# Optimization experiments

Hardware: AMD Instinct MI355X
Metric: run time of the kernel (lower is better)

The kernel has to match this reference:

```python
import jax, jax.numpy as jnp
import numpy as np
import math

B, T, D = 2, 2048, 4096
H, HD = 32, 128  # n_head, head_dim; H*HD == D
THETA = 10000.0


def _rope_tables(T, hd, theta):
    # standard RoPE: freqs_i = theta^(-2i/hd), angle[t,i] = t * freqs_i
    inv = 1.0 / (theta ** (np.arange(0, hd, 2, dtype=np.float32) / hd))  # [hd/2]
    ang = np.arange(T, dtype=np.float32)[:, None] * inv[None, :]          # [T, hd/2]
    return jnp.asarray(np.cos(ang)), jnp.asarray(np.sin(ang))


def setup_inputs() -> dict:
    key = jax.random.key(0)
    ks = jax.random.split(key, 5)
    scale = 1.0 / math.sqrt(D)
    x = jax.random.normal(ks[0], (B, T, D), dtype=jnp.float32)
    Wq = jax.random.normal(ks[1], (D, H * HD), dtype=jnp.float32) * scale
    Wk = jax.random.normal(ks[2], (D, H * HD), dtype=jnp.float32) * scale
    Wv = jax.random.normal(ks[3], (D, H * HD), dtype=jnp.float32) * scale
    Wo = jax.random.normal(ks[4], (D, D), dtype=jnp.float32) * scale
    fc, fs = _rope_tables(T, HD, THETA)
    return {"x": x, "freqs_cos": fc, "freqs_sin": fs,
            "Wq": Wq, "Wk": Wk, "Wv": Wv, "Wo": Wo}


def _apply_rope(t, cos, sin):
    # t: [B, T, H, HD]; complex rotation on interleaved (even, odd) pairs
    tp = t.reshape(*t.shape[:-1], HD // 2, 2)
    xr, xi = tp[..., 0], tp[..., 1]
    c = cos[None, :, None, :]  # [1, T, 1, HD/2]
    s = sin[None, :, None, :]
    out_r = xr * c - xi * s
    out_i = xr * s + xi * c
    return jnp.stack([out_r, out_i], axis=-1).reshape(t.shape)


def reference(x, freqs_cos, freqs_sin, Wq, Wk, Wv, Wo):
    Bc, Tc, _ = x.shape
    q = (x @ Wq).reshape(Bc, Tc, H, HD)
    k = (x @ Wk).reshape(Bc, Tc, H, HD)
    v = (x @ Wv).reshape(Bc, Tc, H, HD)
    q = _apply_rope(q, freqs_cos, freqs_sin)
    k = _apply_rope(k, freqs_cos, freqs_sin)
    scale = 1.0 / math.sqrt(HD)
    scores = jnp.einsum('bqhd,bkhd->bhqk', q, k) * scale  # [B,H,T,T]
    causal = jnp.tril(jnp.ones((Tc, Tc), dtype=bool))
    scores = jnp.where(causal[None, None], scores, -jnp.inf)
    attn = jax.nn.softmax(scores, axis=-1)
    y = jnp.einsum('bhqk,bkhd->bqhd', attn, v).reshape(Bc, Tc, H * HD)
    return y @ Wo
```

## Files before the change

### kernel.cpp

```cpp
#include <hip/hip_runtime.h>

typedef unsigned short ushort_t;
typedef unsigned int uint32;

typedef float f32x4 __attribute__((ext_vector_type(4)));
typedef __bf16 bf16x8 __attribute__((ext_vector_type(8)));
typedef unsigned short us8 __attribute__((ext_vector_type(8)));
typedef unsigned short us4 __attribute__((ext_vector_type(4)));

#define TSEQ 2048
#define DMODEL 4096

__device__ __forceinline__ ushort_t f2bf(float f) {
  uint32 u = __builtin_bit_cast(uint32, f);
  u += 0x7FFFu + ((u >> 16) & 1u);
  return (ushort_t)(u >> 16);
}
__device__ __forceinline__ float bf2f(ushort_t u) {
  return __builtin_bit_cast(float, ((uint32)u) << 16);
}

__device__ __forceinline__ void gload_lds16(const void* g, void* l) {
  auto gp = (const __attribute__((address_space(1))) void*)g;
  auto lp = (__attribute__((address_space(3))) void*)l;
  __builtin_amdgcn_global_load_lds(gp, lp, 16, 0, 0);
}

__global__ __launch_bounds__(256) void k_cast_bf16(const float* __restrict__ in,
                                                   ushort_t* __restrict__ out, int n4) {
  int g = blockIdx.x * 256 + threadIdx.x;
  if (g >= n4) return;
  float4 v = *(const float4*)(in + (size_t)g * 4);
  us4 o; o[0] = f2bf(v.x); o[1] = f2bf(v.y); o[2] = f2bf(v.z); o[3] = f2bf(v.w);
  *(us4*)(out + (size_t)g * 4) = o;
}

__global__ __launch_bounds__(256) void k_transpose_cast4(const float* __restrict__ W0,
                                                         const float* __restrict__ W1,
                                                         const float* __restrict__ W2,
                                                         const float* __restrict__ W3,
                                                         ushort_t* __restrict__ WTbase) {
  __shared__ __align__(16) ushort_t ts[64 * 72];
  const float* Ws[4] = {W0, W1, W2, W3};
  const float* W = Ws[blockIdx.z];
  ushort_t* WT = WTbase + (size_t)blockIdx.z * DMODEL * DMODEL;
  const int tid = threadIdx.x;
  const int n0 = blockIdx.x * 64, k0 = blockIdx.y * 64;
  #pragma unroll
  for (int it = 0; it < 4; ++it) {
    int e = it * 256 + tid;
    int r = e >> 4, c4 = e & 15;
    float4 v = *(const float4*)(W + (size_t)(k0 + r) * DMODEL + n0 + c4 * 4);
    us4 o; o[0] = f2bf(v.x); o[1] = f2bf(v.y); o[2] = f2bf(v.z); o[3] = f2bf(v.w);
    *(us4*)&ts[r * 72 + c4 * 4] = o;
  }
  __syncthreads();
  #pragma unroll
  for (int it = 0; it < 4; ++it) {
    int e = it * 256 + tid;
    int r2 = e >> 4, c4 = e & 15;
    us4 o;
    #pragma unroll
    for (int j = 0; j < 4; ++j) o[j] = ts[(c4 * 4 + j) * 72 + r2];
    *(us4*)(WT + (size_t)(n0 + r2) * DMODEL + k0 + c4 * 4) = o;
  }
}

template <bool OUT_BF16, bool ROPE>
__global__ __launch_bounds__(256, 3)
void k_gemm128(const ushort_t* __restrict__ A, const ushort_t* __restrict__ Bt,
               void* __restrict__ Cv, int M, int N, int K,
               const float* __restrict__ fc, const float* __restrict__ fs) {
  __shared__ __align__(16) ushort_t As[128 * 32];
  __shared__ __align__(16) ushort_t Bs[128 * 32];
  const int tid = threadIdx.x;
  const int w = tid >> 6, l = tid & 63;
  const int wm = w >> 1, wn = w & 1;
  const int lg = l >> 4, lc = l & 15;

  const int nwg = gridDim.x;
  const int cpx = nwg >> 3;
  const int wg = (blockIdx.x & 7) * cpx + (blockIdx.x >> 3);
  const int nbn = N >> 7;
  const int bm = wg / nbn, bn = wg % nbn;

  const ushort_t* Ab = A + (size_t)(bm * 128) * K;
  const ushort_t* Bb = Bt + (size_t)(bn * 128) * K;

  const int csrc = (l & 3) ^ ((l >> 3) & 3);
  const ushort_t* gA[2]; const ushort_t* gB[2];
  int dstOff[2];
  #pragma unroll
  for (int j = 0; j < 2; ++j) {
    int row = w * 32 + j * 16 + (l >> 2);
    gA[j] = Ab + (size_t)row * K + csrc * 8;
    gB[j] = Bb + (size_t)row * K + csrc * 8;
    dstOff[j] = (w * 32 + j * 16) * 32;
  }

  int offA[4], offB[4];
  #pragma unroll
  for (int m = 0; m < 4; ++m)
    offA[m] = (wm * 64 + m * 16 + lc) * 32 + ((lg ^ ((lc >> 1) & 3)) * 8);
  #pragma unroll
  for (int n = 0; n < 4; ++n)
    offB[n] = (wn * 64 + n * 16 + lc) * 32 + ((lg ^ ((lc >> 1) & 3)) * 8);

  f32x4 acc[4][4];
  #pragma unroll
  for (int m = 0; m < 4; ++m)
    #pragma unroll
    for (int n = 0; n < 4; ++n) acc[m][n] = (f32x4){0.f, 0.f, 0.f, 0.f};

  const int NT = K >> 5;
  for (int t = 0; t < NT; ++t) {
    const int k0 = t << 5;
    __syncthreads();
    gload_lds16(gA[0] + k0, &As[dstOff[0]]);
    gload_lds16(gA[1] + k0, &As[dstOff[1]]);
    gload_lds16(gB[0] + k0, &Bs[dstOff[0]]);
    gload_lds16(gB[1] + k0, &Bs[dstOff[1]]);
    asm volatile("s_waitcnt vmcnt(0)" ::: "memory");
    __syncthreads();

    bf16x8 af[4], bfv[4];
    #pragma unroll
    for (int m = 0; m < 4; ++m) af[m] = *(const bf16x8*)&As[offA[m]];
    #pragma unroll
    for (int n = 0; n < 4; ++n) bfv[n] = *(const bf16x8*)&Bs[offB[n]];
    __builtin_amdgcn_s_setprio(1);
    #pragma unroll
    for (int m = 0; m < 4; ++m)
      #pragma unroll
      for (int n = 0; n < 4; ++n)
        acc[m][n] = __builtin_amdgcn_mfma_f32_16x16x32_bf16(af[m], bfv[n], acc[m][n], 0, 0, 0);
    __builtin_amdgcn_s_setprio(0);
  }

  #pragma unroll
  for (int m = 0; m < 4; ++m) {
    int row0 = bm * 128 + wm * 64 + m * 16 + lg * 4;
    #pragma unroll
    for (int n = 0; n < 4; ++n) {
      int col = bn * 128 + wn * 64 + n * 16 + lc;
      if (ROPE) {
        int i0 = (col & 127) >> 1;
        #pragma unroll
        for (int r = 0; r < 4; ++r) {
          int tt = (row0 + r) & (TSEQ - 1);
          float c = fc[tt * 64 + i0];
          float s = fs[tt * 64 + i0];
          float v = acc[m][n][r];
          float p = __shfl_xor(v, 1);
          float ov = (lc & 1) ? (p * s + v * c) : (v * c - p * s);
          ((ushort_t*)Cv)[(size_t)(row0 + r) * N + col] = f2bf(ov);
        }
      } else {
        #pragma unroll
        for (int r = 0; r < 4; ++r) {
          float v = acc[m][n][r];
          if (OUT_BF16) ((ushort_t*)Cv)[(size_t)(row0 + r) * N + col] = f2bf(v);
          else          ((float*)Cv)[(size_t)(row0 + r) * N + col] = v;
        }
      }
    }
  }
}

__global__ __launch_bounds__(512, 2)
void k_attn(const ushort_t* __restrict__ QK, const ushort_t* __restrict__ Vt,
            ushort_t* __restrict__ Y) {
  __shared__ __align__(16) ushort_t Ks[2][64 * 128];
  __shared__ __align__(16) ushort_t Vs[2][128 * 64];
  __shared__ __align__(16) ushort_t Ps[8][16 * 64];
  const int id = blockIdx.x;
  const int xcd = id & 7, slot = id >> 3;
  const int bx = slot & 7, gHi = slot >> 3;
  const int g = gHi * 8 + xcd;
  const int h = g & 31, b = g >> 5;
  const int tid = threadIdx.x;
  const int w = tid >> 6, l = tid & 63;
  const int lg = l >> 4, lc = l & 15;
  const float scale = 0.08838834764831845f;
  const float THR = 8.0f;
  const int QKS = 8192;

  auto stageKV = [&](int kv0, int buf) {
    #pragma unroll
    for (int i = 0; i < 2; ++i) {
      int seg = w * 2 + i;
      {
        int row = seg * 4 + (l >> 4);
        int csrc = (l & 15) ^ (row & 7);
        gload_lds16(QK + (size_t)(b * TSEQ + kv0 + row) * QKS + 4096 + h * 128 + csrc * 8,
                    &Ks[buf][seg * 512]);
      }
      {
        int row = seg * 8 + (l >> 3);
        int csrc = (l & 7) ^ (l >> 3);
        gload_lds16(Vt + (size_t)(h * 128 + row) * DMODEL + b * TSEQ + kv0 + csrc * 8,
                    &Vs[buf][seg * 512]);
      }
    }
  };

  for (int qi = 0; qi < 2; ++qi) {
    const int qt = qi ? (15 - bx) : bx;
    const int q0 = qt * 128;
    const int wrow0 = q0 + w * 16;

    bf16x8 qf[4];
    {
      const ushort_t* qp = QK + (size_t)(b * TSEQ + wrow0 + lc) * QKS + h * 128;
      #pragma unroll
      for (int ks = 0; ks < 4; ++ks) qf[ks] = *(const bf16x8*)(qp + ks * 32 + lg * 8);
    }

    float m_r[4], lp[4];
    #pragma unroll
    for (int r = 0; r < 4; ++r) { m_r[r] = -1e30f; lp[r] = 0.f; }
    f32x4 o[8];
    #pragma unroll
    for (int t = 0; t < 8; ++t) o[t] = (f32x4){0.f, 0.f, 0.f, 0.f};

    const int nkv = (qt + 1) * 2;
    stageKV(0, 0);
    for (int kt = 0; kt < nkv; ++kt) {
      const int cur = kt & 1;
      const int kv0 = kt * 64;
      if (kt + 1 < nkv) {
        stageKV((kt + 1) * 64, cur ^ 1);
        asm volatile("s_waitcnt vmcnt(4)" ::: "memory");
      } else {
        asm volatile("s_waitcnt vmcnt(0)" ::: "memory");
      }
      __builtin_amdgcn_s_barrier();

      if (kv0 <= wrow0 + 15) {
        f32x4 s[4];
        __builtin_amdgcn_s_setprio(1);
        #pragma unroll
        for (int n = 0; n < 4; ++n) {
          s[n] = (f32x4){0.f, 0.f, 0.f, 0.f};
          #pragma unroll
          for (int ks = 0; ks < 4; ++ks) {
            int row = n * 16 + lc;
            bf16x8 kf = *(const bf16x8*)&Ks[cur][row * 128 + ((ks * 32 + lg * 8) ^ ((row & 7) * 8))];
            s[n] = __builtin_amdgcn_mfma_f32_16x16x32_bf16(qf[ks], kf, s[n], 0, 0, 0);
          }
        }
        __builtin_amdgcn_s_setprio(0);

        float sv[4][4];
        if (kv0 + 63 > wrow0) {
          #pragma unroll
          for (int n = 0; n < 4; ++n)
            #pragma unroll
            for (int r = 0; r < 4; ++r) {
              float x = s[n][r] * scale;
              int kvg = kv0 + n * 16 + lc;
              int qg = wrow0 + lg * 4 + r;
              sv[n][r] = (kvg > qg) ? -1e30f : x;
            }
        } else {
          #pragma unroll
          for (int n = 0; n < 4; ++n)
            #pragma unroll
            for (int r = 0; r < 4; ++r) sv[n][r] = s[n][r] * scale;
        }

        float pmax[4];
        #pragma unroll
        for (int r = 0; r < 4; ++r)
          pmax[r] = fmaxf(fmaxf(sv[0][r], sv[1][r]), fmaxf(sv[2][r], sv[3][r]));
        bool ok = (pmax[0] <= m_r[0] + THR) && (pmax[1] <= m_r[1] + THR) &&
                  (pmax[2] <= m_r[2] + THR) && (pmax[3] <= m_r[3] + THR);
        if (!__all(ok)) {
          #pragma unroll
          for (int r = 0; r < 4; ++r) {
            float mx = pmax[r];
            #pragma unroll
            for (int off = 1; off < 16; off <<= 1) mx = fmaxf(mx, __shfl_xor(mx, off, 16));
            float mn = fmaxf(m_r[r], mx);
            float al = __expf(m_r[r] - mn);
            m_r[r] = mn;
            lp[r] *= al;
            #pragma unroll
            for (int t = 0; t < 8; ++t) o[t][r] *= al;
          }
        }

        #pragma unroll
        for (int n = 0; n < 4; ++n)
          #pragma unroll
          for (int r = 0; r < 4; ++r) {
            float p = __expf(sv[n][r] - m_r[r]);
            lp[r] += p;
            int row = lg * 4 + r, col = n * 16 + lc;
            Ps[w][row * 64 + (col ^ (lg * 16))] = f2bf(p);
          }

        __builtin_amdgcn_s_setprio(1);
        #pragma unroll
        for (int kvs = 0; kvs < 2; ++kvs) {
          bf16x8 pa = *(const bf16x8*)&Ps[w][lc * 64 + ((kvs * 32 + lg * 8) ^ ((lc >> 2) * 16))];
          #pragma unroll
          for (int t = 0; t < 8; ++t) {
            int vrow = t * 16 + lc;
            bf16x8 vb = *(const bf16x8*)&Vs[cur][vrow * 64 + ((kvs * 32 + lg * 8) ^ ((vrow & 7) * 8))];
            o[t] = __builtin_amdgcn_mfma_f32_16x16x32_bf16(pa, vb, o[t], 0, 0, 0);
          }
        }
        __builtin_amdgcn_s_setprio(0);
      }
      asm volatile("" ::: "memory");
      __builtin_amdgcn_s_barrier();
    }

    float linv[4];
    #pragma unroll
    for (int r = 0; r < 4; ++r) {
      float ls = lp[r];
      #pragma unroll
      for (int off = 1; off < 16; off <<= 1) ls += __shfl_xor(ls, off, 16);
      linv[r] = 1.0f / ls;
    }

    #pragma unroll
    for (int t = 0; t < 8; ++t)
      #pragma unroll
      for (int r = 0; r < 4; ++r) {
        int row = wrow0 + lg * 4 + r;
        int col = h * 128 + t * 16 + lc;
        Y[(size_t)(b * TSEQ + row) * DMODEL + col] = f2bf(o[t][r] * linv[r]);
      }
  }
}

extern "C" void kernel_launch(void* const* d_in, const int* in_sizes, int n_in,
                              void* d_out, int out_size, void* d_ws, size_t ws_size,
                              hipStream_t stream) {
  const float* x  = (const float*)d_in[0];
  const float* fc = (const float*)d_in[1];
  const float* fs = (const float*)d_in[2];
  const float* Wq = (const float*)d_in[3];
  const float* Wk = (const float*)d_in[4];
  const float* Wv = (const float*)d_in[5];
  const float* Wo = (const float*)d_in[6];

  const size_t SZ = (size_t)4096 * 4096;
  ushort_t* xb  = (ushort_t*)d_ws;
  ushort_t* WqT = xb + SZ;
  ushort_t* WkT = WqT + SZ;
  ushort_t* WvT = WkT + SZ;
  ushort_t* WoT = WvT + SZ;
  ushort_t* qk  = WoT + SZ;
  ushort_t* vT  = qk + 2 * SZ;
  ushort_t* yb  = vT + SZ;

  k_cast_bf16<<<16384, 256, 0, stream>>>(x, xb, 4194304);
  dim3 tg(64, 64, 4);
  k_transpose_cast4<<<tg, 256, 0, stream>>>(Wq, Wk, Wv, Wo, WqT);

  k_gemm128<true, true><<<2048, 256, 0, stream>>>(xb, WqT, qk, 4096, 8192, 4096, fc, fs);
  k_gemm128<true, false><<<1024, 256, 0, stream>>>(WvT, xb, vT, 4096, 4096, 4096, nullptr, nullptr);

  k_attn<<<512, 512, 0, stream>>>(qk, vT, yb);

  k_gemm128<false, false><<<1024, 256, 0, stream>>>(yb, WoT, d_out, 4096, 4096, 4096, nullptr, nullptr);
}
```

Before: 914.5 us.

## Double-buffer GEMM LDS with 128x256 tiles, 512 threads, split Q/K outputs

The GEMM kernel now uses 512-thread blocks computing 128x256 tiles with double-buffered LDS. The next K-slice load is issued before the current slice's MFMAs, so each iteration needs one barrier instead of two. The LDS swizzle also changes. The fused Q/K projection is split into two separate launches writing separate Q and K buffers, and the attention QK^T loop is reordered to iterate ks outermost. The aim is to hide global-load latency and raise data reuse per block, at the cost of more LDS per block and more launches.

```diff
diff --git a/kernel.cpp b/kernel.cpp
--- a/kernel.cpp
+++ b/kernel.cpp
@@ -67,67 +67,74 @@
 }
 
 template <bool OUT_BF16, bool ROPE>
-__global__ __launch_bounds__(256, 3)
-void k_gemm128(const ushort_t* __restrict__ A, const ushort_t* __restrict__ Bt,
-               void* __restrict__ Cv, int M, int N, int K,
-               const float* __restrict__ fc, const float* __restrict__ fs) {
-  __shared__ __align__(16) ushort_t As[128 * 32];
-  __shared__ __align__(16) ushort_t Bs[128 * 32];
+__global__ __launch_bounds__(512, 4)
+void k_gemm(const ushort_t* __restrict__ A, const ushort_t* __restrict__ Bt,
+            void* __restrict__ Cv, int M, int N, int K,
+            const float* __restrict__ fc, const float* __restrict__ fs) {
+  __shared__ __align__(16) ushort_t As[2][128 * 32];
+  __shared__ __align__(16) ushort_t Bs[2][256 * 32];
   const int tid = threadIdx.x;
   const int w = tid >> 6, l = tid & 63;
-  const int wm = w >> 1, wn = w & 1;
+  const int wr = w >> 2, wc = w & 3;
   const int lg = l >> 4, lc = l & 15;
 
   const int nwg = gridDim.x;
   const int cpx = nwg >> 3;
   const int wg = (blockIdx.x & 7) * cpx + (blockIdx.x >> 3);
-  const int nbn = N >> 7;
+  const int nbn = N >> 8;
   const int bm = wg / nbn, bn = wg % nbn;
 
   const ushort_t* Ab = A + (size_t)(bm * 128) * K;
-  const ushort_t* Bb = Bt + (size_t)(bn * 128) * K;
-
-  const int csrc = (l & 3) ^ ((l >> 3) & 3);
-  const ushort_t* gA[2]; const ushort_t* gB[2];
-  int dstOff[2];
-  #pragma unroll
-  for (int j = 0; j < 2; ++j) {
-    int row = w * 32 + j * 16 + (l >> 2);
-    gA[j] = Ab + (size_t)row * K + csrc * 8;
-    gB[j] = Bb + (size_t)row * K + csrc * 8;
-    dstOff[j] = (w * 32 + j * 16) * 32;
-  }
-
+  const ushort_t* Bb = Bt + (size_t)(bn * 256) * K;
+
+  const int slotA = tid;
+  const int rowA = slotA >> 2;
+  const int chA = (slotA & 3) ^ (rowA & 3) ^ (2 * ((rowA >> 2) & 1));
+  const ushort_t* gAp = Ab + (size_t)rowA * K + chA * 8;
+  const int dstA = (w * 64) * 8;
+
+  const int rowB0 = tid >> 2, rowB1 = (512 + tid) >> 2;
+  const int chB0 = (tid & 3) ^ (rowB0 & 3) ^ (2 * ((rowB0 >> 2) & 1));
+  const int chB1 = (tid & 3) ^ (rowB1 & 3) ^ (2 * ((rowB1 >> 2) & 1));
+  const ushort_t* gBp0 = Bb + (size_t)rowB0 * K + chB0 * 8;
+  const ushort_t* gBp1 = Bb + (size_t)rowB1 * K + chB1 * 8;
+  const int dstB0 = (w * 64) * 8;
+  const int dstB1 = (512 + w * 64) * 8;
+
+  const int rswz = (lg ^ (lc & 3) ^ (2 * ((lc >> 2) & 1))) * 8;
   int offA[4], offB[4];
   #pragma unroll
+  for (int m = 0; m < 4; ++m) offA[m] = (wr * 64 + m * 16 + lc) * 32 + rswz;
+  #pragma unroll
+  for (int n = 0; n < 4; ++n) offB[n] = (wc * 64 + n * 16 + lc) * 32 + rswz;
+
+  f32x4 acc[4][4];
+  #pragma unroll
   for (int m = 0; m < 4; ++m)
-    offA[m] = (wm * 64 + m * 16 + lc) * 32 + ((lg ^ ((lc >> 1) & 3)) * 8);
-  #pragma unroll
-  for (int n = 0; n < 4; ++n)
-    offB[n] = (wn * 64 + n * 16 + lc) * 32 + ((lg ^ ((lc >> 1) & 3)) * 8);
-
-  f32x4 acc[4][4];
-  #pragma unroll
-  for (int m = 0; m < 4; ++m)
     #pragma unroll
     for (int n = 0; n < 4; ++n) acc[m][n] = (f32x4){0.f, 0.f, 0.f, 0.f};
 
   const int NT = K >> 5;
+  auto stage = [&](int t, int buf) {
+    const int k0 = t << 5;
+    gload_lds16(gAp + k0, &As[buf][dstA]);
+    gload_lds16(gBp0 + k0, &Bs[buf][dstB0]);
+    gload_lds16(gBp1 + k0, &Bs[buf][dstB1]);
+  };
+
+  stage(0, 0);
+  asm volatile("s_waitcnt vmcnt(0)" ::: "memory");
+  __builtin_amdgcn_s_barrier();
+
   for (int t = 0; t < NT; ++t) {
-    const int k0 = t << 5;
-    __syncthreads();
-    gload_lds16(gA[0] + k0, &As[dstOff[0]]);
-    gload_lds16(gA[1] + k0, &As[dstOff[1]]);
-    gload_lds16(gB[0] + k0, &Bs[dstOff[0]]);
-    gload_lds16(gB[1] + k0, &Bs[dstOff[1]]);
-    asm volatile("s_waitcnt vmcnt(0)" ::: "memory");
-    __syncthreads();
+    const int cur = t & 1;
+    if (t + 1 < NT) stage(t + 1, cur ^ 1);
 
     bf16x8 af[4], bfv[4];
     #pragma unroll
-    for (int m = 0; m < 4; ++m) af[m] = *(const bf16x8*)&As[offA[m]];
-    #pragma unroll
-    for (int n = 0; n < 4; ++n) bfv[n] = *(const bf16x8*)&Bs[offB[n]];
+    for (int m = 0; m < 4; ++m) af[m] = *(const bf16x8*)&As[cur][offA[m]];
+    #pragma unroll
+    for (int n = 0; n < 4; ++n) bfv[n] = *(const bf16x8*)&Bs[cur][offB[n]];
     __builtin_amdgcn_s_setprio(1);
     #pragma unroll
     for (int m = 0; m < 4; ++m)
@@ -135,14 +142,19 @@
       for (int n = 0; n < 4; ++n)
         acc[m][n] = __builtin_amdgcn_mfma_f32_16x16x32_bf16(af[m], bfv[n], acc[m][n], 0, 0, 0);
     __builtin_amdgcn_s_setprio(0);
+
+    if (t + 1 < NT) {
+      asm volatile("s_waitcnt vmcnt(0)" ::: "memory");
+      __builtin_amdgcn_s_barrier();
+    }
   }
 
   #pragma unroll
   for (int m = 0; m < 4; ++m) {
-    int row0 = bm * 128 + wm * 64 + m * 16 + lg * 4;
+    int row0 = bm * 128 + wr * 64 + m * 16 + lg * 4;
     #pragma unroll
     for (int n = 0; n < 4; ++n) {
-      int col = bn * 128 + wn * 64 + n * 16 + lc;
+      int col = bn * 256 + wc * 64 + n * 16 + lc;
       if (ROPE) {
         int i0 = (col & 127) >> 1;
         #pragma unroll
@@ -168,8 +180,8 @@
 }
 
 __global__ __launch_bounds__(512, 2)
-void k_attn(const ushort_t* __restrict__ QK, const ushort_t* __restrict__ Vt,
-            ushort_t* __restrict__ Y) {
+void k_attn(const ushort_t* __restrict__ Q, const ushort_t* __restrict__ Kb,
+            const ushort_t* __restrict__ Vt, ushort_t* __restrict__ Y) {
   __shared__ __align__(16) ushort_t Ks[2][64 * 128];
   __shared__ __align__(16) ushort_t Vs[2][128 * 64];
   __shared__ __align__(16) ushort_t Ps[8][16 * 64];
@@ -183,7 +195,6 @@
   const int lg = l >> 4, lc = l & 15;
   const float scale = 0.08838834764831845f;
   const float THR = 8.0f;
-  const int QKS = 8192;
 
   auto stageKV = [&](int kv0, int buf) {
     #pragma unroll
@@ -192,7 +203,7 @@
       {
         int row = seg * 4 + (l >> 4);
         int csrc = (l & 15) ^ (row & 7);
-        gload_lds16(QK + (size_t)(b * TSEQ + kv0 + row) * QKS + 4096 + h * 128 + csrc * 8,
+        gload_lds16(Kb + (size_t)(b * TSEQ + kv0 + row) * DMODEL + h * 128 + csrc * 8,
                     &Ks[buf][seg * 512]);
       }
       {
@@ -211,7 +222,7 @@
 
     bf16x8 qf[4];
     {
-      const ushort_t* qp = QK + (size_t)(b * TSEQ + wrow0 + lc) * QKS + h * 128;
+      const ushort_t* qp = Q + (size_t)(b * TSEQ + wrow0 + lc) * DMODEL + h * 128;
       #pragma unroll
       for (int ks = 0; ks < 4; ++ks) qf[ks] = *(const bf16x8*)(qp + ks * 32 + lg * 8);
     }
@@ -238,17 +249,17 @@
 
       if (kv0 <= wrow0 + 15) {
         f32x4 s[4];
+        #pragma unroll
+        for (int n = 0; n < 4; ++n) s[n] = (f32x4){0.f, 0.f, 0.f, 0.f};
         __builtin_amdgcn_s_setprio(1);
         #pragma unroll
-        for (int n = 0; n < 4; ++n) {
-          s[n] = (f32x4){0.f, 0.f, 0.f, 0.f};
-          #pragma unroll
-          for (int ks = 0; ks < 4; ++ks) {
+        for (int ks = 0; ks < 4; ++ks)
+          #pragma unroll
+          for (int n = 0; n < 4; ++n) {
             int row = n * 16 + lc;
             bf16x8 kf = *(const bf16x8*)&Ks[cur][row * 128 + ((ks * 32 + lg * 8) ^ ((row & 7) * 8))];
             s[n] = __builtin_amdgcn_mfma_f32_16x16x32_bf16(qf[ks], kf, s[n], 0, 0, 0);
           }
-        }
         __builtin_amdgcn_s_setprio(0);
 
         float sv[4][4];
@@ -354,18 +365,20 @@
   ushort_t* WkT = WqT + SZ;
   ushort_t* WvT = WkT + SZ;
   ushort_t* WoT = WvT + SZ;
-  ushort_t* qk  = WoT + SZ;
-  ushort_t* vT  = qk + 2 * SZ;
+  ushort_t* qb  = WoT + SZ;
+  ushort_t* kb  = qb + SZ;
+  ushort_t* vT  = kb + SZ;
   ushort_t* yb  = vT + SZ;
 
   k_cast_bf16<<<16384, 256, 0, stream>>>(x, xb, 4194304);
   dim3 tg(64, 64, 4);
   k_transpose_cast4<<<tg, 256, 0, stream>>>(Wq, Wk, Wv, Wo, WqT);
 
-  k_gemm128<true, true><<<2048, 256, 0, stream>>>(xb, WqT, qk, 4096, 8192, 4096, fc, fs);
-  k_gemm128<true, false><<<1024, 256, 0, stream>>>(WvT, xb, vT, 4096, 4096, 4096, nullptr, nullptr);
-
-  k_attn<<<512, 512, 0, stream>>>(qk, vT, yb);
-
-  k_gemm128<false, false><<<1024, 256, 0, stream>>>(yb, WoT, d_out, 4096, 4096, 4096, nullptr, nullptr);
-}
+  k_gemm<true, true><<<512, 512, 0, stream>>>(xb, WqT, qb, 4096, 4096, 4096, fc, fs);
+  k_gemm<true, true><<<512, 512, 0, stream>>>(xb, WkT, kb, 4096, 4096, 4096, fc, fs);
+  k_gemm<true, false><<<512, 512, 0, stream>>>(WvT, xb, vT, 4096, 4096, 4096, nullptr, nullptr);
+
+  k_attn<<<512, 512, 0, stream>>>(qb, kb, vT, yb);
+
+  k_gemm<false, false><<<512, 512, 0, stream>>>(yb, WoT, d_out, 4096, 4096, 4096, nullptr, nullptr);
+}
```

New measurement: 798.1 us. 1.15x faster.
